# Performance work log

Hardware: AMD Instinct MI355X
Metric: run time of the kernel (lower is better)

Reference implementation:

```python
import jax, jax.numpy as jnp
import numpy as np

N_NODES = 100000
N_EDGES = 1600000
IN_DIM = 75
H_COMP = 64
H_BOND = 16
DEPTH = 3


def setup_inputs() -> dict:
    key = jax.random.key(0)
    ks = jax.random.split(key, 8)
    x = jax.random.normal(ks[0], (N_NODES, IN_DIM), dtype=jnp.float32)
    edge_index = jax.random.randint(ks[1], (2, N_EDGES), 0, N_NODES, dtype=jnp.int64)
    edge_attr = jax.random.normal(ks[2], (N_EDGES, H_BOND), dtype=jnp.float32)
    proj_w = jax.random.normal(ks[3], (IN_DIM, H_COMP), dtype=jnp.float32) * (1.0 / np.sqrt(IN_DIM))
    proj_b = jnp.zeros((H_COMP,), dtype=jnp.float32)
    u2_w = jax.random.normal(ks[4], (DEPTH, H_COMP + H_BOND, H_COMP), dtype=jnp.float32) * (1.0 / np.sqrt(H_COMP + H_BOND))
    u2_b = jnp.zeros((DEPTH, H_COMP), dtype=jnp.float32)
    u1_w = jax.random.normal(ks[5], (DEPTH, 2 * H_COMP, H_COMP), dtype=jnp.float32) * (1.0 / np.sqrt(2 * H_COMP))
    u1_b = jnp.zeros((DEPTH, H_COMP), dtype=jnp.float32)
    return {"x": x, "edge_index": edge_index, "edge_attr": edge_attr,
            "proj_w": proj_w, "proj_b": proj_b,
            "u2_w": u2_w, "u2_b": u2_b, "u1_w": u1_w, "u1_b": u1_b}


def reference(x, edge_index, edge_attr, proj_w, proj_b, u2_w, u2_b, u1_w, u1_b):
    # PyG default flow source_to_target: messages gathered from edge_index[0],
    # scatter-added at edge_index[1].
    src, dst = edge_index[0], edge_index[1]
    n = x.shape[0]
    # input projection: [N, in_dim] -> [N, H]
    h = x @ proj_w + proj_b
    for l in range(u2_w.shape[0]):
        # message: concat(x_j, edge_attr) -> Linear -> LeakyReLU(0.1)   [E, H+B] -> [E, H]
        z = jnp.concatenate([h[src], edge_attr], axis=-1)
        m = jax.nn.leaky_relu(z @ u2_w[l] + u2_b[l], negative_slope=0.1)
        # aggregate: scatter-add over destination nodes  [E, H] -> [N, H]
        agg = jax.ops.segment_sum(m, dst, num_segments=n)
        # update: concat(x, agg) -> Linear  [N, 2H] -> [N, H]
        h = jnp.concatenate([h, agg], axis=-1) @ u1_w[l] + u1_b[l]
    return h
```

## Files before the change

kernel.cpp:

```cpp
#include <hip/hip_runtime.h>

typedef __attribute__((ext_vector_type(8))) short frag_ab;
typedef __attribute__((ext_vector_type(4))) float frag_cd;
typedef __attribute__((ext_vector_type(4))) short short4v;

__device__ __forceinline__ short f2bf(float f) {
  union { float f; unsigned u; } v; v.f = f;
  unsigned r = v.u + 0x7fffu + ((v.u >> 16) & 1u);
  return (short)(r >> 16);
}

__global__ void wconv(const float* __restrict__ W, short* __restrict__ out,
                      int Keff, int S, int nmat)
{
  int tid = blockIdx.x * 256 + threadIdx.x;
  int per = S * 4 * 64;
  if (tid >= nmat * per) return;
  int m = tid / per, r = tid % per;
  int s = r / 256, ct = (r >> 6) & 3, ln = r & 63;
  const float* Wm = W + (size_t)m * Keff * 64;
  __align__(16) short tmp[8];
  for (int j = 0; j < 8; ++j) {
    int k = s * 32 + (ln >> 4) * 8 + j;
    int n = ct * 16 + (ln & 15);
    tmp[j] = (k < Keff) ? f2bf(Wm[k * 64 + n]) : (short)0;
  }
  *(uint4*)&out[((size_t)m * per + (size_t)(s * 4 + ct) * 64 + ln) * 8] = *(uint4*)tmp;
}

#define AS1 104
__global__ __launch_bounds__(256, 4) void proj_kernel(
    const float* __restrict__ x, const short* __restrict__ wt,
    const float* __restrict__ bias, short* __restrict__ hbf, int N)
{
  __shared__ __align__(16) short A[128 * AS1];
  int t = threadIdx.x;
  int nb = blockIdx.x * 128;
  int ln = t & 63;
  frag_ab bf[12];
  for (int s = 0; s < 3; ++s)
    for (int ct = 0; ct < 4; ++ct)
      bf[s * 4 + ct] = *(const frag_ab*)&wt[((size_t)(s * 4 + ct) * 64 + ln) * 8];
  for (int i = 0; i < 48; ++i) {
    int q = i * 256 + t; int el = q / 96; int c = q - el * 96;
    int rg = nb + el;
    float v = (c < 75 && rg < N) ? x[rg * 75 + c] : 0.f;
    A[el * AS1 + c] = f2bf(v);
  }
  __syncthreads();
  int wv = t >> 6;
  int lrow = ln & 15, lk = ln >> 4;
  frag_cd acc[2][4];
  for (int rt = 0; rt < 2; ++rt) for (int ct = 0; ct < 4; ++ct) {
    frag_cd z = {0.f, 0.f, 0.f, 0.f}; acc[rt][ct] = z;
  }
  for (int s = 0; s < 3; ++s) {
    frag_ab a0 = *(const frag_ab*)&A[(wv*32 + lrow) * AS1 + s*32 + lk*8];
    frag_ab a1 = *(const frag_ab*)&A[(wv*32 + 16 + lrow) * AS1 + s*32 + lk*8];
    for (int ct = 0; ct < 4; ++ct) {
      acc[0][ct] = __builtin_amdgcn_mfma_f32_16x16x32_bf16(a0, bf[s*4+ct], acc[0][ct], 0, 0, 0);
      acc[1][ct] = __builtin_amdgcn_mfma_f32_16x16x32_bf16(a1, bf[s*4+ct], acc[1][ct], 0, 0, 0);
    }
  }
  float bv[4];
  for (int ct = 0; ct < 4; ++ct) bv[ct] = bias[ct*16 + lrow];
  for (int rt = 0; rt < 2; ++rt)
    for (int ct = 0; ct < 4; ++ct)
      for (int r = 0; r < 4; ++r) {
        int row = wv*32 + rt*16 + lk*4 + r;
        int rg = nb + row;
        if (rg < N) hbf[(size_t)rg * 64 + ct*16 + lrow] = f2bf(acc[rt][ct][r] + bv[ct]);
      }
}

__global__ __launch_bounds__(256) void hist_kernel(
    const int* __restrict__ dst, int* __restrict__ counts, int E)
{
  int i = blockIdx.x * 256 + threadIdx.x;
  if (i < E) atomicAdd(&counts[dst[i]], 1);
}

#define SCAN_TILE 2048
__global__ __launch_bounds__(256) void scan_k1(
    const int* __restrict__ counts, int* __restrict__ offsets,
    int* __restrict__ bsum, int n)
{
  __shared__ int ts[256];
  int t = threadIdx.x;
  int base = blockIdx.x * SCAN_TILE + t * 8;
  int v[8]; int s = 0;
  for (int j = 0; j < 8; ++j) { v[j] = (base + j < n) ? counts[base + j] : 0; s += v[j]; }
  ts[t] = s; __syncthreads();
  for (int off = 1; off < 256; off <<= 1) {
    int x = (t >= off) ? ts[t - off] : 0;
    __syncthreads();
    ts[t] += x;
    __syncthreads();
  }
  if (t == 255) bsum[blockIdx.x] = ts[255];
  int run = (t > 0) ? ts[t - 1] : 0;
  for (int j = 0; j < 8; ++j) { if (base + j < n) offsets[base + j] = run; run += v[j]; }
}

__global__ void scan_k2(int* bsum, int nb) {
  if (threadIdx.x == 0 && blockIdx.x == 0) {
    int run = 0;
    for (int b = 0; b < nb; ++b) { int x = bsum[b]; bsum[b] = run; run += x; }
  }
}

__global__ __launch_bounds__(256) void scan_k3(
    int* __restrict__ offsets, const int* __restrict__ bsum, int n)
{
  int add = bsum[blockIdx.x];
  int base = blockIdx.x * SCAN_TILE + threadIdx.x;
  for (int j = 0; j < 8; ++j) { int i = base + j * 256; if (i < n) offsets[i] += add; }
}

__global__ __launch_bounds__(256) void scatter_kernel(
    const int* __restrict__ src, const int* __restrict__ dst,
    const float* __restrict__ attr, int* __restrict__ offsets,
    int* __restrict__ srcs, int* __restrict__ dsts,
    short* __restrict__ attr_s, int E)
{
  int e = blockIdx.x * 256 + threadIdx.x;
  if (e < E) {
    int d = dst[e];
    int p = atomicAdd(&offsets[d], 1);
    srcs[p] = src[e];
    dsts[p] = d;
    __align__(16) short tmp[16];
    for (int c = 0; c < 16; ++c) tmp[c] = f2bf(attr[(size_t)e * 16 + c]);
    *(uint4*)&attr_s[(size_t)p * 16]     = *(uint4*)&tmp[0];
    *(uint4*)&attr_s[(size_t)p * 16 + 8] = *(uint4*)&tmp[8];
  }
}

__global__ __launch_bounds__(256) void masks_kernel(
    const int* __restrict__ dsts, uint2* __restrict__ masks, int E, int W)
{
  int w = blockIdx.x * 256 + threadIdx.x;
  if (w >= W) return;
  int base = w * 32;
  unsigned em = 0, cm = 0;
  int dprev = (base < E) ? dsts[base] : -1;
  int a = 0;
  for (int i = 1; i <= 32; ++i) {
    int d = (i < 32) ? ((base + i < E) ? dsts[base + i] : -1) : -2;
    if (d != dprev) {
      int end = i - 1;
      em |= 1u << end;
      if (a > 0 && end < 31) cm |= 1u << end;
      a = i; dprev = d;
    }
  }
  masks[w] = make_uint2(em, cm);
}

#define MS 66
__global__ __launch_bounds__(256, 4) void msg_kernel(
    const short* __restrict__ hbf, const short* __restrict__ attr_s,
    const int* __restrict__ srcs, const int* __restrict__ dsts,
    const short* __restrict__ wt, const float* __restrict__ bias,
    const uint2* __restrict__ masks, float* __restrict__ agg, int E)
{
  __shared__ __align__(16) char u[128 * MS * 4];
  __shared__ int dstl[128];
  short* A = (short*)u;
  float* M = (float*)u;

  int t = threadIdx.x;
  int eb = blockIdx.x * 128;
  int ln = t & 63;

  if (t < 128) dstl[t] = (eb + t < E) ? dsts[eb + t] : -1;

  frag_ab bf[12];
  for (int s = 0; s < 3; ++s)
    for (int ct = 0; ct < 4; ++ct)
      bf[s * 4 + ct] = *(const frag_ab*)&wt[((size_t)(s * 4 + ct) * 64 + ln) * 8];

  for (int i = 0; i < 4; ++i) {
    int q = i * 256 + t; int el = q >> 3; int c = q & 7;
    int p = eb + el;
    int s = (p < E) ? srcs[p] : 0;
    *(uint4*)&A[el * AS1 + c * 8] = *(const uint4*)&hbf[(size_t)s * 64 + c * 8];
  }
  {
    int el = t >> 1, c = t & 1;
    int p = eb + el;
    uint4 v = {0u, 0u, 0u, 0u};
    if (p < E) v = *(const uint4*)&attr_s[(size_t)p * 16 + c * 8];
    *(uint4*)&A[el * AS1 + 64 + c * 8] = v;
    uint4 z = {0u, 0u, 0u, 0u};
    *(uint4*)&A[el * AS1 + 80 + c * 8] = z;
  }
  __syncthreads();

  int wv = t >> 6;
  int lrow = ln & 15, lk = ln >> 4;
  frag_cd acc[2][4];
  for (int rt = 0; rt < 2; ++rt) for (int ct = 0; ct < 4; ++ct) {
    frag_cd z = {0.f, 0.f, 0.f, 0.f}; acc[rt][ct] = z;
  }
  for (int s = 0; s < 3; ++s) {
    frag_ab a0 = *(const frag_ab*)&A[(wv*32 + lrow) * AS1 + s*32 + lk*8];
    frag_ab a1 = *(const frag_ab*)&A[(wv*32 + 16 + lrow) * AS1 + s*32 + lk*8];
    for (int ct = 0; ct < 4; ++ct) {
      acc[0][ct] = __builtin_amdgcn_mfma_f32_16x16x32_bf16(a0, bf[s*4+ct], acc[0][ct], 0, 0, 0);
      acc[1][ct] = __builtin_amdgcn_mfma_f32_16x16x32_bf16(a1, bf[s*4+ct], acc[1][ct], 0, 0, 0);
    }
  }
  float bv[4];
  for (int ct = 0; ct < 4; ++ct) bv[ct] = bias[ct*16 + lrow];

  __syncthreads();
  for (int rt = 0; rt < 2; ++rt)
    for (int ct = 0; ct < 4; ++ct)
      for (int r = 0; r < 4; ++r) {
        int row = wv*32 + rt*16 + lk*4 + r;
        float m = acc[rt][ct][r] + bv[ct];
        m = m > 0.f ? m : 0.1f * m;
        M[row * MS + ct*16 + lrow] = m;
      }
  __syncthreads();

  {
    uint2 mk = masks[blockIdx.x * 4 + wv];
    unsigned em = __builtin_amdgcn_readfirstlane(mk.x);
    unsigned cm = __builtin_amdgcn_readfirstlane(mk.y);
    float s = 0.f;
#pragma unroll
    for (int i = 0; i < 32; ++i) {
      s += M[(wv*32 + i) * MS + ln];
      if ((em >> i) & 1u) {
        int d = __builtin_amdgcn_readfirstlane(dstl[wv*32 + i]);
        if (d >= 0) {
          float* dest = &agg[(size_t)d * 64 + ln];
          if ((cm >> i) & 1u) *dest = s;
          else unsafeAtomicAdd(dest, s);
        }
        s = 0.f;
      }
    }
  }
}

#define AS2 136
__global__ __launch_bounds__(256, 4) void upd_kernel(
    const short* __restrict__ hbf, const float* __restrict__ agg,
    const short* __restrict__ wt, const float* __restrict__ bias,
    float* __restrict__ hout, short* __restrict__ hbfo, int N, int last)
{
  __shared__ __align__(16) short A[128 * AS2];
  int t = threadIdx.x;
  int nb = blockIdx.x * 128;
  int ln = t & 63;
  for (int i = 0; i < 4; ++i) {
    int q = i * 256 + t; int el = q >> 3; int c = q & 7;
    int rg = nb + el;
    uint4 v = {0u, 0u, 0u, 0u};
    if (rg < N) v = *(const uint4*)&hbf[(size_t)rg * 64 + c * 8];
    *(uint4*)&A[el * AS2 + c * 8] = v;
  }
  for (int i = 0; i < 8; ++i) {
    int q = i * 256 + t; int el = q >> 4; int c = q & 15;
    int rg = nb + el;
    float4 v = make_float4(0.f, 0.f, 0.f, 0.f);
    if (rg < N) v = *(const float4*)&agg[(size_t)rg * 64 + c * 4];
    short4v s4 = { f2bf(v.x), f2bf(v.y), f2bf(v.z), f2bf(v.w) };
    *(short4v*)&A[el * AS2 + 64 + c * 4] = s4;
  }
  __syncthreads();
  int wv = t >> 6;
  int lrow = ln & 15, lk = ln >> 4;
  frag_cd acc[2][4];
  for (int rt = 0; rt < 2; ++rt) for (int ct = 0; ct < 4; ++ct) {
    frag_cd z = {0.f, 0.f, 0.f, 0.f}; acc[rt][ct] = z;
  }
  for (int s = 0; s < 4; ++s) {
    frag_ab a0 = *(const frag_ab*)&A[(wv*32 + lrow) * AS2 + s*32 + lk*8];
    frag_ab a1 = *(const frag_ab*)&A[(wv*32 + 16 + lrow) * AS2 + s*32 + lk*8];
    for (int ct = 0; ct < 4; ++ct) {
      frag_ab b = *(const frag_ab*)&wt[((size_t)(s * 4 + ct) * 64 + ln) * 8];
      acc[0][ct] = __builtin_amdgcn_mfma_f32_16x16x32_bf16(a0, b, acc[0][ct], 0, 0, 0);
      acc[1][ct] = __builtin_amdgcn_mfma_f32_16x16x32_bf16(a1, b, acc[1][ct], 0, 0, 0);
    }
  }
  float bv[4];
  for (int ct = 0; ct < 4; ++ct) bv[ct] = bias[ct*16 + lrow];
  for (int rt = 0; rt < 2; ++rt)
    for (int ct = 0; ct < 4; ++ct)
      for (int r = 0; r < 4; ++r) {
        int row = wv*32 + rt*16 + lk*4 + r;
        int rg = nb + row;
        if (rg < N) {
          float v = acc[rt][ct][r] + bv[ct];
          if (last) hout[(size_t)rg * 64 + ct*16 + lrow] = v;
          hbfo[(size_t)rg * 64 + ct*16 + lrow] = f2bf(v);
        }
      }
}

extern "C" void kernel_launch(void* const* d_in, const int* in_sizes, int n_in,
                              void* d_out, int out_size, void* d_ws, size_t ws_size,
                              hipStream_t stream) {
  const float* x    = (const float*)d_in[0];
  const int*   ei   = (const int*)d_in[1];
  const float* attr = (const float*)d_in[2];
  const float* pw   = (const float*)d_in[3];
  const float* pb   = (const float*)d_in[4];
  const float* u2w  = (const float*)d_in[5];
  const float* u2b  = (const float*)d_in[6];
  const float* u1w  = (const float*)d_in[7];
  const float* u1b  = (const float*)d_in[8];

  const int N = in_sizes[0] / 75;
  const int E = in_sizes[1] / 2;
  const int* src = ei;
  const int* dst = ei + E;

  float* hout = (float*)d_out;
  char*  ws   = (char*)d_ws;
  size_t nh   = (size_t)N * 64;
  size_t off  = 0;
  short* hbf   = (short*)(ws + off); off += nh * 2;
  float* agg   = (float*)(ws + off); off += nh * 4;
  int*   srcs  = (int*)  (ws + off); off += (size_t)E * 4;
  int*   dsts  = (int*)  (ws + off); off += (size_t)E * 4;
  short* attr_s= (short*)(ws + off); off += (size_t)E * 32;
  const int EB = (E + 127) / 128;
  uint2* masks = (uint2*)(ws + off); off += (size_t)EB * 4 * 8;
  short* projt = (short*)(ws + off); off += 3 * 4 * 64 * 8 * 2;
  short* u2t   = (short*)(ws + off); off += (size_t)3 * 3 * 4 * 64 * 8 * 2;
  short* u1t   = (short*)(ws + off); off += (size_t)3 * 4 * 4 * 64 * 8 * 2;
  int* counts  = (int*)agg;
  int* offsets = counts + N;
  int* bsum    = offsets + N;

  const int NB = (N + 127) / 128;
  const int GE = (E + 255) / 256;
  const int NS = (N + SCAN_TILE - 1) / SCAN_TILE;
  const int NW = EB * 4;

  wconv<<<3, 256, 0, stream>>>(pw, projt, 75, 3, 1);
  wconv<<<9, 256, 0, stream>>>(u2w, u2t, 80, 3, 3);
  wconv<<<12, 256, 0, stream>>>(u1w, u1t, 128, 4, 3);
  proj_kernel<<<NB, 256, 0, stream>>>(x, projt, pb, hbf, N);
  hipMemsetAsync(counts, 0, (size_t)N * 4, stream);
  hist_kernel<<<GE, 256, 0, stream>>>(dst, counts, E);
  scan_k1<<<NS, 256, 0, stream>>>(counts, offsets, bsum, N);
  scan_k2<<<1, 64, 0, stream>>>(bsum, NS);
  scan_k3<<<NS, 256, 0, stream>>>(offsets, bsum, N);
  scatter_kernel<<<GE, 256, 0, stream>>>(src, dst, attr, offsets, srcs, dsts, attr_s, E);
  masks_kernel<<<(NW + 255) / 256, 256, 0, stream>>>(dsts, masks, E, NW);

  for (int l = 0; l < 3; ++l) {
    hipMemsetAsync(agg, 0, nh * 4, stream);
    msg_kernel<<<EB, 256, 0, stream>>>(hbf, attr_s, srcs, dsts,
                                       u2t + (size_t)l * 6144, u2b + l * 64,
                                       masks, agg, E);
    upd_kernel<<<NB, 256, 0, stream>>>(hbf, agg,
                                       u1t + (size_t)l * 8192, u1b + l * 64,
                                       hout, hbf, N, l == 2);
  }
}
```

Baseline: 751.8 us.

## Split edge sort into permutation scatter plus coalesced gather; fuse mask build; drop per-layer memsets

The atomic scatter now writes only an edge index permutation. A separate gather kernel reads src, dst and attr through that permutation and writes the sorted arrays with coalesced stores. The same kernel builds the segment masks with a wave ballot, which removes masks_kernel. The update kernel zeroes agg after reading it, so the per-layer memset is replaced by a single initial memset, at the cost of extra stores and an extra launch.

```diff
diff --git a/kernel.cpp b/kernel.cpp
--- a/kernel.cpp
+++ b/kernel.cpp
@@ -117,44 +117,50 @@
   for (int j = 0; j < 8; ++j) { int i = base + j * 256; if (i < n) offsets[i] += add; }
 }
 
-__global__ __launch_bounds__(256) void scatter_kernel(
-    const int* __restrict__ src, const int* __restrict__ dst,
-    const float* __restrict__ attr, int* __restrict__ offsets,
-    int* __restrict__ srcs, int* __restrict__ dsts,
-    short* __restrict__ attr_s, int E)
+__global__ __launch_bounds__(256) void perm_scatter(
+    const int* __restrict__ dst, int* __restrict__ offsets,
+    int* __restrict__ perm, int E)
 {
   int e = blockIdx.x * 256 + threadIdx.x;
   if (e < E) {
-    int d = dst[e];
-    int p = atomicAdd(&offsets[d], 1);
+    int p = atomicAdd(&offsets[dst[e]], 1);
+    perm[p] = e;
+  }
+}
+
+__global__ __launch_bounds__(256) void gather_permute(
+    const int* __restrict__ perm, const int* __restrict__ src,
+    const int* __restrict__ dst, const float* __restrict__ attr,
+    int* __restrict__ srcs, int* __restrict__ dsts,
+    short* __restrict__ attr_s, uint2* __restrict__ masks, int E, int NW)
+{
+  int p = blockIdx.x * 256 + threadIdx.x;
+  int d = -1;
+  if (p < E) {
+    int e = perm[p];
+    d = dst[e];
     srcs[p] = src[e];
     dsts[p] = d;
+    const float4* a4 = (const float4*)(attr + (size_t)e * 16);
+    float4 v0 = a4[0], v1 = a4[1], v2 = a4[2], v3 = a4[3];
     __align__(16) short tmp[16];
-    for (int c = 0; c < 16; ++c) tmp[c] = f2bf(attr[(size_t)e * 16 + c]);
+    tmp[0]=f2bf(v0.x); tmp[1]=f2bf(v0.y); tmp[2]=f2bf(v0.z); tmp[3]=f2bf(v0.w);
+    tmp[4]=f2bf(v1.x); tmp[5]=f2bf(v1.y); tmp[6]=f2bf(v1.z); tmp[7]=f2bf(v1.w);
+    tmp[8]=f2bf(v2.x); tmp[9]=f2bf(v2.y); tmp[10]=f2bf(v2.z); tmp[11]=f2bf(v2.w);
+    tmp[12]=f2bf(v3.x); tmp[13]=f2bf(v3.y); tmp[14]=f2bf(v3.z); tmp[15]=f2bf(v3.w);
     *(uint4*)&attr_s[(size_t)p * 16]     = *(uint4*)&tmp[0];
     *(uint4*)&attr_s[(size_t)p * 16 + 8] = *(uint4*)&tmp[8];
   }
-}
-
-__global__ __launch_bounds__(256) void masks_kernel(
-    const int* __restrict__ dsts, uint2* __restrict__ masks, int E, int W)
-{
-  int w = blockIdx.x * 256 + threadIdx.x;
-  if (w >= W) return;
-  int base = w * 32;
-  unsigned em = 0, cm = 0;
-  int dprev = (base < E) ? dsts[base] : -1;
-  int a = 0;
-  for (int i = 1; i <= 32; ++i) {
-    int d = (i < 32) ? ((base + i < E) ? dsts[base + i] : -1) : -2;
-    if (d != dprev) {
-      int end = i - 1;
-      em |= 1u << end;
-      if (a > 0 && end < 31) cm |= 1u << end;
-      a = i; dprev = d;
-    }
-  }
-  masks[w] = make_uint2(em, cm);
+  int dnext = __shfl_down(d, 1);
+  bool end = ((p & 31) == 31) || (d != dnext);
+  unsigned long long bm = __ballot(end);
+  int lw = threadIdx.x & 63;
+  if (lw == 0 || lw == 32) {
+    unsigned em = (lw == 0) ? (unsigned)bm : (unsigned)(bm >> 32);
+    unsigned cm = em & ~(em & (~em + 1u)) & 0x7fffffffu;
+    int w = p >> 5;
+    if (w < NW) masks[w] = make_uint2(em, cm);
+  }
 }
 
 #define MS 66
@@ -248,7 +254,7 @@
 
 #define AS2 136
 __global__ __launch_bounds__(256, 4) void upd_kernel(
-    const short* __restrict__ hbf, const float* __restrict__ agg,
+    const short* __restrict__ hbf, float* __restrict__ agg,
     const short* __restrict__ wt, const float* __restrict__ bias,
     float* __restrict__ hout, short* __restrict__ hbfo, int N, int last)
 {
@@ -267,7 +273,13 @@
     int q = i * 256 + t; int el = q >> 4; int c = q & 15;
     int rg = nb + el;
     float4 v = make_float4(0.f, 0.f, 0.f, 0.f);
-    if (rg < N) v = *(const float4*)&agg[(size_t)rg * 64 + c * 4];
+    if (rg < N) {
+      v = *(const float4*)&agg[(size_t)rg * 64 + c * 4];
+      if (!last) {
+        float4 z = make_float4(0.f, 0.f, 0.f, 0.f);
+        *(float4*)&agg[(size_t)rg * 64 + c * 4] = z;
+      }
+    }
     short4v s4 = { f2bf(v.x), f2bf(v.y), f2bf(v.z), f2bf(v.w) };
     *(short4v*)&A[el * AS2 + 64 + c * 4] = s4;
   }
@@ -328,6 +340,7 @@
   float* agg   = (float*)(ws + off); off += nh * 4;
   int*   srcs  = (int*)  (ws + off); off += (size_t)E * 4;
   int*   dsts  = (int*)  (ws + off); off += (size_t)E * 4;
+  int*   perm  = (int*)  (ws + off); off += (size_t)E * 4;
   short* attr_s= (short*)(ws + off); off += (size_t)E * 32;
   const int EB = (E + 127) / 128;
   uint2* masks = (uint2*)(ws + off); off += (size_t)EB * 4 * 8;
@@ -342,6 +355,7 @@
   const int GE = (E + 255) / 256;
   const int NS = (N + SCAN_TILE - 1) / SCAN_TILE;
   const int NW = EB * 4;
+  const int GP = (NW * 32 + 255) / 256;
 
   wconv<<<3, 256, 0, stream>>>(pw, projt, 75, 3, 1);
   wconv<<<9, 256, 0, stream>>>(u2w, u2t, 80, 3, 3);
@@ -352,11 +366,12 @@
   scan_k1<<<NS, 256, 0, stream>>>(counts, offsets, bsum, N);
   scan_k2<<<1, 64, 0, stream>>>(bsum, NS);
   scan_k3<<<NS, 256, 0, stream>>>(offsets, bsum, N);
-  scatter_kernel<<<GE, 256, 0, stream>>>(src, dst, attr, offsets, srcs, dsts, attr_s, E);
-  masks_kernel<<<(NW + 255) / 256, 256, 0, stream>>>(dsts, masks, E, NW);
-
+  perm_scatter<<<GE, 256, 0, stream>>>(dst, offsets, perm, E);
+  gather_permute<<<GP, 256, 0, stream>>>(perm, src, dst, attr,
+                                         srcs, dsts, attr_s, masks, E, NW);
+
+  hipMemsetAsync(agg, 0, nh * 4, stream);
   for (int l = 0; l < 3; ++l) {
-    hipMemsetAsync(agg, 0, nh * 4, stream);
     msg_kernel<<<EB, 256, 0, stream>>>(hbf, attr_s, srcs, dsts,
                                        u2t + (size_t)l * 6144, u2b + l * 64,
                                        masks, agg, E);
```

Result: slower. 826.6 us (+10.0%).
